# Kernel tuning notes

Measured on AMD Instinct MI355X. Metric: run time of the kernel, lower is better.

Reference implementation:

```python
import jax, jax.numpy as jnp
import numpy as np

ADAPTER_RATIO = 0.2


def setup_inputs() -> dict:
    key = jax.random.key(0)
    k1, k2, k3, k4, k5 = jax.random.split(key, 5)
    B, D, R, N_DOM, N_TXT = 16384, 1024, 256, 3, 1380
    image_features = jax.random.normal(k1, (B, D), dtype=jnp.float32)
    domain_labels = jax.random.randint(k2, (B,), 0, N_DOM, dtype=jnp.int64)
    W1 = jax.random.normal(k3, (N_DOM, D, R), dtype=jnp.float32) * 0.02
    W2 = jax.random.normal(k4, (N_DOM, R, D), dtype=jnp.float32) * 0.02
    txt = jax.random.normal(k5, (N_TXT, D), dtype=jnp.float32)
    # text features are L2-normalized at module init (encode_text then norm)
    text_features = txt / jnp.linalg.norm(txt, axis=-1, keepdims=True)
    logit_scale = jnp.asarray(np.log(1.0 / 0.07), dtype=jnp.float32)  # CLIP init
    return {
        "image_features": image_features,
        "domain_labels": domain_labels,
        "W1": W1,
        "W2": W2,
        "text_features": text_features,
        "logit_scale": logit_scale,
    }


def reference(image_features, domain_labels, W1, W2, text_features, logit_scale):
    # Domain-routed adapter MLP: run all n_domains experts (n is tiny), then
    # select the routed output per sample (equivalent to the per-sample loop).
    h = jax.nn.relu(jnp.einsum("bd,ndr->bnr", image_features, W1))  # [B,n,R]
    a = jax.nn.relu(jnp.einsum("bnr,nrd->bnd", h, W2))              # [B,n,D]
    idx = domain_labels[:, None, None]                                # [B,1,1]
    adapter_features = jnp.take_along_axis(a, idx, axis=1)[:, 0, :]   # [B,D]
    fused = ADAPTER_RATIO * adapter_features + (1.0 - ADAPTER_RATIO) * image_features
    fused = fused / jnp.linalg.norm(fused, axis=-1, keepdims=True)
    # text_features already normalized; concat over domains done upstream: [N_TXT, D]
    logits = jnp.exp(logit_scale) * (fused @ text_features.T)         # [B, N_TXT]
    return logits
```

## Files before the change

### kernel.cpp

```cpp
#include <hip/hip_runtime.h>
#include <hip/hip_bf16.h>
#include <math.h>

using bf16 = __hip_bfloat16;
typedef __attribute__((ext_vector_type(8))) short bf16x8;
typedef __attribute__((ext_vector_type(4))) float f32x4;
typedef __attribute__((ext_vector_type(4))) unsigned short us4;

#define GAS __attribute__((address_space(1)))
#define LAS __attribute__((address_space(3)))

__device__ __forceinline__ void gload_lds16(const bf16* g, bf16* lds) {
  __builtin_amdgcn_global_load_lds((const GAS void*)g, (LAS void*)lds, 16, 0, 0);
}
__device__ __forceinline__ float b2f(unsigned short u) {
  union { unsigned short s; bf16 b; } x; x.s = u; return __bfloat162float(x.b);
}

__global__ __launch_bounds__(256) void hist_k(const int* __restrict__ lab,
                                              int* __restrict__ blockHist) {
  const int blk = blockIdx.x, t = threadIdx.x;
  const int lane = t & 63, w = t >> 6;
  const int d = lab[blk * 256 + t];
  __shared__ int wc[4][3];
#pragma unroll
  for (int dd = 0; dd < 3; ++dd) {
    unsigned long long m = __ballot(d == dd);
    if (lane == 0) wc[w][dd] = __popcll(m);
  }
  __syncthreads();
  if (t < 3) blockHist[blk * 3 + t] = wc[0][t] + wc[1][t] + wc[2][t] + wc[3][t];
}

__global__ __launch_bounds__(256) void scan_k(const int* __restrict__ blockHist,
                                              int* __restrict__ blockOff,
                                              int* __restrict__ meta) {
  __shared__ int h[64][3];
  __shared__ int tot[3];
  const int t = threadIdx.x;
  if (t < 192) h[t / 3][t % 3] = blockHist[t];
  __syncthreads();
  if (t < 3) {
    int s = 0;
    for (int b = 0; b < 64; ++b) { int v = h[b][t]; h[b][t] = s; s += v; }
    tot[t] = s;
    meta[t] = s;
  }
  __syncthreads();
  if (t == 0) { meta[4] = 0; meta[5] = tot[0]; meta[6] = tot[0] + tot[1]; }
  if (t < 192) {
    int b = t / 3, d = t % 3;
    int base = (d == 0) ? 0 : (d == 1 ? tot[0] : tot[0] + tot[1]);
    blockOff[t] = base + h[b][d];
  }
}

__global__ __launch_bounds__(256) void scatter2_k(const int* __restrict__ lab,
                                                  const int* __restrict__ blockOff,
                                                  int* __restrict__ perm,
                                                  int* __restrict__ iperm) {
  const int blk = blockIdx.x, t = threadIdx.x;
  const int lane = t & 63, w = t >> 6;
  const int i = blk * 256 + t;
  const int d = lab[i];
  __shared__ int wc[4][3];
  unsigned long long mymask = 0;
#pragma unroll
  for (int dd = 0; dd < 3; ++dd) {
    unsigned long long m = __ballot(d == dd);
    if (lane == 0) wc[w][dd] = __popcll(m);
    if (dd == d) mymask = m;
  }
  __syncthreads();
  int woff = 0;
  for (int ww = 0; ww < w; ++ww) woff += wc[ww][d];
  const unsigned long long lt = ((unsigned long long)1 << lane) - 1;
  const int rank = blockOff[blk * 3 + d] + woff + __popcll(mymask & lt);
  perm[rank] = i;
  iperm[i] = rank;
}

__global__ __launch_bounds__(256) void cvt_all_k(const float* __restrict__ x,
                                                 const float* __restrict__ txt,
                                                 const int* __restrict__ iperm,
                                                 bf16* __restrict__ Xbc,
                                                 bf16* __restrict__ Tb) {
  const int nx = 16384 * 1024 / 4;
  const int ntext = 1536 * 1024;
  const int total = nx + ntext;
  for (int i = blockIdx.x * 256 + threadIdx.x; i < total; i += 2048 * 256) {
    if (i < nx) {
      const int row = i >> 8, c4 = i & 255;
      float4 v = ((const float4*)x)[i];
      bf16 t[4] = {__float2bfloat16(v.x), __float2bfloat16(v.y),
                   __float2bfloat16(v.z), __float2bfloat16(v.w)};
      ((us4*)Xbc)[(size_t)iperm[row] * 256 + c4] = *(const us4*)t;
    } else {
      int jj = i - nx;
      Tb[jj] = (jj < 1380 * 1024) ? __float2bfloat16(txt[jj]) : __float2bfloat16(0.f);
    }
  }
}

__global__ __launch_bounds__(256) void tr_wt_k(const float* __restrict__ W1,
                                               const float* __restrict__ W2,
                                               bf16* __restrict__ W1T,
                                               bf16* __restrict__ W2T) {
  __shared__ float s[64][65];
  int b = blockIdx.x;
  const float* W; bf16* WT; int R, C;
  if (b < 192) { W = W1; WT = W1T; R = 1024; C = 256; }
  else         { b -= 192; W = W2; WT = W2T; R = 256; C = 1024; }
  const int d = b / 64, tb = b % 64;
  const int tilesPerRow = C / 64;
  const int r0 = (tb / tilesPerRow) * 64;
  const int c0 = (tb % tilesPerRow) * 64;
  const float* Wd = W + (size_t)d * R * C;
  bf16* WTd = WT + (size_t)d * R * C;
  const int tx = threadIdx.x & 63, ty = threadIdx.x >> 6;
#pragma unroll
  for (int i = 0; i < 16; ++i)
    s[ty + i * 4][tx] = Wd[(size_t)(r0 + ty + i * 4) * C + c0 + tx];
  __syncthreads();
#pragma unroll
  for (int i = 0; i < 16; ++i)
    WTd[(size_t)(c0 + ty + i * 4) * R + r0 + tx] = __float2bfloat16(s[tx][ty + i * 4]);
}

template <int EPI, int NBLK>
__global__ __launch_bounds__(256) void gemm_bt(
    const bf16* __restrict__ A, const bf16* __restrict__ BT, bf16* __restrict__ Cv,
    const int* __restrict__ meta, int N, int K, int ldc, int Nvalid,
    const bf16* __restrict__ xb, float* __restrict__ ssp) {
  const int bid = blockIdx.x;
  const int xcd = bid & 7;
  const int seq = bid >> 3;
  const int nblkidx = seq % NBLK;
  const int dm = xcd + 8 * (seq / NBLK);
  const int dom = dm >> 7;
  const int mblk = dm & 127;

  const int cnt = meta[dom];
  const int base = meta[4 + dom];
  BT += (size_t)dom * N * K;

  const int m0 = mblk * 128;
  if (m0 >= cnt) return;
  const int n0 = nblkidx * 128;

  __shared__ bf16 sA[2][128][32];
  __shared__ bf16 sB[2][128][32];

  const int tid = threadIdx.x;
  const int wid = tid >> 6;
  const int lane = tid & 63;

  const int srow = (wid << 4) + (lane >> 2);
  const int skoff = (((lane & 3) ^ ((lane >> 2) & 3)) << 3);

  int p0 = m0 + srow;       if (p0 > cnt - 1) p0 = cnt - 1;
  int p1 = m0 + srow + 64;  if (p1 > cnt - 1) p1 = cnt - 1;
  const bf16* a0 = A + (size_t)(base + p0) * K + skoff;
  const bf16* a1 = A + (size_t)(base + p1) * K + skoff;
  const bf16* b0 = BT + (size_t)(n0 + srow) * K + skoff;
  const bf16* b1 = BT + (size_t)(n0 + srow + 64) * K + skoff;

  const int fr = lane & 15;
  const int fq = lane >> 4;
  const int rchunk = (fq ^ (fr & 3)) << 3;

  f32x4 acc[4][4];
#pragma unroll
  for (int m = 0; m < 4; ++m)
#pragma unroll
    for (int n = 0; n < 4; ++n) acc[m][n] = (f32x4){0.f, 0.f, 0.f, 0.f};

  const int nk = K >> 5;
  auto stage = [&](int buf, int kt) {
    gload_lds16(a0 + kt * 32, &sA[buf][wid * 16][0]);
    gload_lds16(a1 + kt * 32, &sA[buf][wid * 16 + 64][0]);
    gload_lds16(b0 + kt * 32, &sB[buf][wid * 16][0]);
    gload_lds16(b1 + kt * 32, &sB[buf][wid * 16 + 64][0]);
  };

  stage(0, 0);
  __syncthreads();
  const int wr = wid >> 1, wc = wid & 1;
  for (int kt = 0; kt < nk; ++kt) {
    const int cur = kt & 1;
    if (kt + 1 < nk) stage(cur ^ 1, kt + 1);
    bf16x8 af[4], bfr[4];
#pragma unroll
    for (int m = 0; m < 4; ++m)
      af[m] = *(const bf16x8*)&sA[cur][wr * 64 + m * 16 + fr][rchunk];
#pragma unroll
    for (int n = 0; n < 4; ++n)
      bfr[n] = *(const bf16x8*)&sB[cur][wc * 64 + n * 16 + fr][rchunk];
#pragma unroll
    for (int m = 0; m < 4; ++m)
#pragma unroll
      for (int n = 0; n < 4; ++n)
        acc[m][n] = __builtin_amdgcn_mfma_f32_16x16x32_bf16(af[m], bfr[n], acc[m][n], 0, 0, 0);
    __syncthreads();
  }

  if (EPI == 0) {
#pragma unroll
    for (int m = 0; m < 4; ++m) {
#pragma unroll
      for (int r = 0; r < 4; ++r) {
        const int p = m0 + wr * 64 + m * 16 + fq * 4 + r;
        if (p < cnt) {
          const size_t crow = (size_t)(base + p);
#pragma unroll
          for (int n = 0; n < 4; ++n) {
            const int col = n0 + wc * 64 + n * 16 + fr;
            if (col < Nvalid)
              Cv[crow * (size_t)ldc + col] = __float2bfloat16(fmaxf(acc[m][n][r], 0.f));
          }
        }
      }
    }
  } else {
    __shared__ float ssred[128][2];
#pragma unroll
    for (int m = 0; m < 4; ++m) {
#pragma unroll
      for (int r = 0; r < 4; ++r) {
        const int lr = wr * 64 + m * 16 + fq * 4 + r;
        const int p = m0 + lr;
        float rowss = 0.f;
        if (p < cnt) {
          const size_t crow = (size_t)(base + p);
#pragma unroll
          for (int n = 0; n < 4; ++n) {
            const int col = n0 + wc * 64 + n * 16 + fr;
            const float g = 0.2f * fmaxf(acc[m][n][r], 0.f) +
                            0.8f * b2f(*(const unsigned short*)&xb[crow * 1024 + col]);
            Cv[crow * (size_t)ldc + col] = __float2bfloat16(g);
            rowss += g * g;
          }
        }
        rowss += __shfl_xor(rowss, 1, 16);
        rowss += __shfl_xor(rowss, 2, 16);
        rowss += __shfl_xor(rowss, 4, 16);
        rowss += __shfl_xor(rowss, 8, 16);
        if (fr == 0) ssred[lr][wc] = rowss;
      }
    }
    __syncthreads();
    if (tid < 128) {
      const int p = m0 + tid;
      if (p < cnt)
        ssp[(size_t)nblkidx * 16384 + base + p] = ssred[tid][0] + ssred[tid][1];
    }
  }
}

__global__ __launch_bounds__(256, 2) void gemm3_cnt(
    const bf16* __restrict__ A, const bf16* __restrict__ BT,
    float* __restrict__ C, const float* __restrict__ scale_ptr,
    const float* __restrict__ ssp, const int* __restrict__ perm) {
  extern __shared__ bf16 smem[];
  bf16* sA0 = smem;
  bf16* sB0 = smem + 16384;

  const int tid = threadIdx.x;
  const int lane = tid & 63, wid = tid >> 6;
  const int wr = wid >> 1, wc = wid & 1;
  const int fr = lane & 15, fq = lane >> 4;

  const int bid = blockIdx.x;
  const int x = bid & 7, seq = bid >> 3;
  const int mb = x * 16 + (seq >> 3), nb = seq & 7;
  const int m0 = mb << 7, n0 = nb * 192;

  auto STAGE = [&](int t) {
    const int s = t & 1, koff = t << 6;
    bf16* da = sA0 + (s << 13);
#pragma unroll
    for (int L = 0; L < 4; ++L) {
      const int idx = (L << 8) + tid;
      const int r = idx >> 3, c = idx & 7;
      gload_lds16(A + (size_t)(m0 + r) * 1024 + koff + ((c ^ (r & 7)) << 3),
                  da + ((idx & ~63) << 3));
    }
    bf16* db = sB0 + s * 12288;
#pragma unroll
    for (int L = 0; L < 6; ++L) {
      const int idx = (L << 8) + tid;
      const int r = idx >> 3, c = idx & 7;
      gload_lds16(BT + (size_t)(n0 + r) * 1024 + koff + ((c ^ (r & 7)) << 3),
                  db + ((idx & ~63) << 3));
    }
  };
  auto LDA = [&](int s, int kk, bf16x8* dst) {
    const bf16* base = sA0 + (s << 13);
#pragma unroll
    for (int m = 0; m < 4; ++m) {
      const int row = (wr << 6) + (m << 4) + fr;
      dst[m] = *(const bf16x8*)(base + (row << 6) + ((((kk << 2) + fq) ^ (fr & 7)) << 3));
    }
  };
  auto LDB = [&](int s, int kk, bf16x8* dst) {
    const bf16* base = sB0 + s * 12288;
#pragma unroll
    for (int n = 0; n < 6; ++n) {
      const int row = wc * 96 + (n << 4) + fr;
      dst[n] = *(const bf16x8*)(base + (row << 6) + ((((kk << 2) + fq) ^ (fr & 7)) << 3));
    }
  };

  f32x4 acc[4][6];
#pragma unroll
  for (int m = 0; m < 4; ++m)
#pragma unroll
    for (int n = 0; n < 6; ++n) acc[m][n] = (f32x4){0.f, 0.f, 0.f, 0.f};

  STAGE(0); STAGE(1);
  asm volatile("s_waitcnt vmcnt(10)" ::: "memory");
  __builtin_amdgcn_s_barrier();

  const int nt = 16;
  for (int t = 0; t < nt; ++t) {
    const int s = t & 1;
    bf16x8 a0[4], a1[4], b0[6], b1[6];
    LDA(s, 0, a0); LDB(s, 0, b0);
    LDA(s, 1, a1); LDB(s, 1, b1);
    asm volatile("s_waitcnt lgkmcnt(0)" ::: "memory");
    __builtin_amdgcn_sched_barrier(0);
    __builtin_amdgcn_s_barrier();
    __builtin_amdgcn_sched_barrier(0);
    if (t + 2 < nt) STAGE(t + 2);
    __builtin_amdgcn_s_setprio(1);
#pragma unroll
    for (int m = 0; m < 4; ++m)
#pragma unroll
      for (int n = 0; n < 6; ++n)
        acc[m][n] = __builtin_amdgcn_mfma_f32_16x16x32_bf16(a0[m], b0[n], acc[m][n], 0, 0, 0);
#pragma unroll
    for (int m = 0; m < 4; ++m)
#pragma unroll
      for (int n = 0; n < 6; ++n)
        acc[m][n] = __builtin_amdgcn_mfma_f32_16x16x32_bf16(a1[m], b1[n], acc[m][n], 0, 0, 0);
    __builtin_amdgcn_s_setprio(0);
    if (t + 2 < nt) {
      asm volatile("s_waitcnt vmcnt(10)" ::: "memory");
    } else if (t + 1 < nt) {
      asm volatile("s_waitcnt vmcnt(0)" ::: "memory");
    }
    __builtin_amdgcn_sched_barrier(0);
    __builtin_amdgcn_s_barrier();
    __builtin_amdgcn_sched_barrier(0);
  }

  float* rlds = (float*)smem;
  int*   plds = (int*)((char*)smem + 512);
  if (tid < 128) {
    float s = 0.f;
#pragma unroll
    for (int b = 0; b < 8; ++b) s += ssp[b * 16384 + m0 + tid];
    rlds[tid] = rsqrtf(s);
    plds[tid] = perm[m0 + tid];
  }
  __syncthreads();

  const float sc = expf(*scale_ptr);
#pragma unroll
  for (int m = 0; m < 4; ++m) {
    const int lrow = (wr << 6) + (m << 4) + (fq << 2);
#pragma unroll
    for (int r = 0; r < 4; ++r) {
      const float rv = sc * rlds[lrow + r];
      const size_t orow = (size_t)plds[lrow + r];
#pragma unroll
      for (int n = 0; n < 6; ++n) {
        const int gcol = n0 + wc * 96 + (n << 4) + fr;
        if (gcol < 1380) C[orow * 1380 + gcol] = acc[m][n][r] * rv;
      }
    }
  }
}

extern "C" void kernel_launch(void* const* d_in, const int* in_sizes, int n_in,
                              void* d_out, int out_size, void* d_ws, size_t ws_size,
                              hipStream_t stream) {
  (void)in_sizes; (void)n_in; (void)out_size; (void)ws_size;
  const float* x    = (const float*)d_in[0];
  const int*   lab  = (const int*)d_in[1];
  const float* W1   = (const float*)d_in[2];
  const float* W2   = (const float*)d_in[3];
  const float* text = (const float*)d_in[4];
  const float* lsc  = (const float*)d_in[5];
  float* out = (float*)d_out;

  const int B = 16384, D = 1024, R = 256, NTP = 1536;

  char* p = (char*)d_ws;
  auto carve = [&](size_t bytes) {
    char* r = p;
    p += (bytes + 255) & ~(size_t)255;
    return r;
  };
  int*   meta  = (int*)carve(64);
  int*   bhist = (int*)carve(64 * 3 * 4);
  int*   boff  = (int*)carve(64 * 3 * 4);
  int*   perm  = (int*)carve((size_t)B * 4);
  int*   iperm = (int*)carve((size_t)B * 4);
  float* ssp   = (float*)carve((size_t)8 * B * 4);
  bf16*  Xbc   = (bf16*)carve((size_t)B * D * 2);
  bf16*  W1T   = (bf16*)carve((size_t)3 * R * D * 2);
  bf16*  W2T   = (bf16*)carve((size_t)3 * D * R * 2);
  bf16*  Tb    = (bf16*)carve((size_t)NTP * D * 2);
  bf16*  H     = (bf16*)carve((size_t)B * R * 2);
  bf16*  Fbc   = (bf16*)carve((size_t)B * D * 2);

  hist_k<<<B / 256, 256, 0, stream>>>(lab, bhist);
  scan_k<<<1, 256, 0, stream>>>(bhist, boff, meta);
  scatter2_k<<<B / 256, 256, 0, stream>>>(lab, boff, perm, iperm);

  cvt_all_k<<<2048, 256, 0, stream>>>(x, text, iperm, Xbc, Tb);
  tr_wt_k<<<384, 256, 0, stream>>>(W1, W2, W1T, W2T);

  gemm_bt<0, 2><<<768, 256, 0, stream>>>(
      Xbc, W1T, H, meta, R, D, R, R, nullptr, nullptr);
  gemm_bt<1, 8><<<3072, 256, 0, stream>>>(
      H, W2T, Fbc, meta, D, R, D, D, Xbc, ssp);
  gemm3_cnt<<<1024, 256, 81920, stream>>>(Fbc, Tb, out, lsc, ssp, perm);
}
```

Measured before the change: 154.5 us.

## Merge weight transpose into conversion kernel and widen GEMM K-tile to 64

Folds the weight transpose kernel into the input/text conversion kernel, so one launch does both and the per-launch overhead and serialization gap go away. Makes the K-tile of the grouped adapter GEMMs a template parameter and sets it to 64. The LDS staging and XOR swizzle are generalized to the wider tile, and each synchronized step now issues two MFMA sub-steps. The aim is fewer barriers and more work per pipeline stage, at the cost of twice the LDS per block, which may reduce occupancy.

Result: no change. 152.1 us (-1.5%).

```diff
diff --git a/kernel.cpp b/kernel.cpp
--- a/kernel.cpp
+++ b/kernel.cpp
@@ -80,15 +80,41 @@
   iperm[i] = rank;
 }
 
-__global__ __launch_bounds__(256) void cvt_all_k(const float* __restrict__ x,
-                                                 const float* __restrict__ txt,
-                                                 const int* __restrict__ iperm,
-                                                 bf16* __restrict__ Xbc,
-                                                 bf16* __restrict__ Tb) {
+__global__ __launch_bounds__(256) void prep_k(const float* __restrict__ x,
+                                              const float* __restrict__ txt,
+                                              const float* __restrict__ W1,
+                                              const float* __restrict__ W2,
+                                              const int* __restrict__ iperm,
+                                              bf16* __restrict__ Xbc,
+                                              bf16* __restrict__ Tb,
+                                              bf16* __restrict__ W1T,
+                                              bf16* __restrict__ W2T) {
+  __shared__ float s[64][65];
+  if (blockIdx.x < 384) {
+    int b = blockIdx.x;
+    const float* W; bf16* WT; int R, C;
+    if (b < 192) { W = W1; WT = W1T; R = 1024; C = 256; }
+    else         { b -= 192; W = W2; WT = W2T; R = 256; C = 1024; }
+    const int d = b / 64, tb = b % 64;
+    const int tilesPerRow = C / 64;
+    const int r0 = (tb / tilesPerRow) * 64;
+    const int c0 = (tb % tilesPerRow) * 64;
+    const float* Wd = W + (size_t)d * R * C;
+    bf16* WTd = WT + (size_t)d * R * C;
+    const int tx = threadIdx.x & 63, ty = threadIdx.x >> 6;
+#pragma unroll
+    for (int i = 0; i < 16; ++i)
+      s[ty + i * 4][tx] = Wd[(size_t)(r0 + ty + i * 4) * C + c0 + tx];
+    __syncthreads();
+#pragma unroll
+    for (int i = 0; i < 16; ++i)
+      WTd[(size_t)(c0 + ty + i * 4) * R + r0 + tx] = __float2bfloat16(s[tx][ty + i * 4]);
+    return;
+  }
   const int nx = 16384 * 1024 / 4;
   const int ntext = 1536 * 1024;
   const int total = nx + ntext;
-  for (int i = blockIdx.x * 256 + threadIdx.x; i < total; i += 2048 * 256) {
+  for (int i = (blockIdx.x - 384) * 256 + threadIdx.x; i < total; i += 2048 * 256) {
     if (i < nx) {
       const int row = i >> 8, c4 = i & 255;
       float4 v = ((const float4*)x)[i];
@@ -102,32 +128,7 @@
   }
 }
 
-__global__ __launch_bounds__(256) void tr_wt_k(const float* __restrict__ W1,
-                                               const float* __restrict__ W2,
-                                               bf16* __restrict__ W1T,
-                                               bf16* __restrict__ W2T) {
-  __shared__ float s[64][65];
-  int b = blockIdx.x;
-  const float* W; bf16* WT; int R, C;
-  if (b < 192) { W = W1; WT = W1T; R = 1024; C = 256; }
-  else         { b -= 192; W = W2; WT = W2T; R = 256; C = 1024; }
-  const int d = b / 64, tb = b % 64;
-  const int tilesPerRow = C / 64;
-  const int r0 = (tb / tilesPerRow) * 64;
-  const int c0 = (tb % tilesPerRow) * 64;
-  const float* Wd = W + (size_t)d * R * C;
-  bf16* WTd = WT + (size_t)d * R * C;
-  const int tx = threadIdx.x & 63, ty = threadIdx.x >> 6;
-#pragma unroll
-  for (int i = 0; i < 16; ++i)
-    s[ty + i * 4][tx] = Wd[(size_t)(r0 + ty + i * 4) * C + c0 + tx];
-  __syncthreads();
-#pragma unroll
-  for (int i = 0; i < 16; ++i)
-    WTd[(size_t)(c0 + ty + i * 4) * R + r0 + tx] = __float2bfloat16(s[tx][ty + i * 4]);
-}
-
-template <int EPI, int NBLK>
+template <int EPI, int NBLK, int BK>
 __global__ __launch_bounds__(256) void gemm_bt(
     const bf16* __restrict__ A, const bf16* __restrict__ BT, bf16* __restrict__ Cv,
     const int* __restrict__ meta, int N, int K, int ldc, int Nvalid,
@@ -148,26 +149,34 @@
   if (m0 >= cnt) return;
   const int n0 = nblkidx * 128;
 
-  __shared__ bf16 sA[2][128][32];
-  __shared__ bf16 sB[2][128][32];
+  constexpr int CH = BK / 8;
+  __shared__ bf16 sA[2][128][BK];
+  __shared__ bf16 sB[2][128][BK];
 
   const int tid = threadIdx.x;
   const int wid = tid >> 6;
   const int lane = tid & 63;
-
-  const int srow = (wid << 4) + (lane >> 2);
-  const int skoff = (((lane & 3) ^ ((lane >> 2) & 3)) << 3);
-
-  int p0 = m0 + srow;       if (p0 > cnt - 1) p0 = cnt - 1;
-  int p1 = m0 + srow + 64;  if (p1 > cnt - 1) p1 = cnt - 1;
-  const bf16* a0 = A + (size_t)(base + p0) * K + skoff;
-  const bf16* a1 = A + (size_t)(base + p1) * K + skoff;
-  const bf16* b0 = BT + (size_t)(n0 + srow) * K + skoff;
-  const bf16* b1 = BT + (size_t)(n0 + srow + 64) * K + skoff;
-
   const int fr = lane & 15;
   const int fq = lane >> 4;
-  const int rchunk = (fq ^ (fr & 3)) << 3;
+
+  auto stage = [&](int buf, int kt) {
+    const int koff = kt * BK;
+#pragma unroll
+    for (int L = 0; L < CH / 2; ++L) {
+      const int idx = L * 256 + tid;
+      const int r = idx / CH, c = idx % CH;
+      int ar = m0 + r; if (ar > cnt - 1) ar = cnt - 1;
+      gload_lds16(A + (size_t)(base + ar) * K + koff + ((c ^ (r & (CH - 1))) << 3),
+                  &sA[buf][0][0] + ((idx & ~63) << 3));
+    }
+#pragma unroll
+    for (int L = 0; L < CH / 2; ++L) {
+      const int idx = L * 256 + tid;
+      const int r = idx / CH, c = idx % CH;
+      gload_lds16(BT + (size_t)(n0 + r) * K + koff + ((c ^ (r & (CH - 1))) << 3),
+                  &sB[buf][0][0] + ((idx & ~63) << 3));
+    }
+  };
 
   f32x4 acc[4][4];
 #pragma unroll
@@ -175,32 +184,29 @@
 #pragma unroll
     for (int n = 0; n < 4; ++n) acc[m][n] = (f32x4){0.f, 0.f, 0.f, 0.f};
 
-  const int nk = K >> 5;
-  auto stage = [&](int buf, int kt) {
-    gload_lds16(a0 + kt * 32, &sA[buf][wid * 16][0]);
-    gload_lds16(a1 + kt * 32, &sA[buf][wid * 16 + 64][0]);
-    gload_lds16(b0 + kt * 32, &sB[buf][wid * 16][0]);
-    gload_lds16(b1 + kt * 32, &sB[buf][wid * 16 + 64][0]);
-  };
-
+  const int nk = K / BK;
   stage(0, 0);
   __syncthreads();
   const int wr = wid >> 1, wc = wid & 1;
   for (int kt = 0; kt < nk; ++kt) {
     const int cur = kt & 1;
     if (kt + 1 < nk) stage(cur ^ 1, kt + 1);
-    bf16x8 af[4], bfr[4];
-#pragma unroll
-    for (int m = 0; m < 4; ++m)
-      af[m] = *(const bf16x8*)&sA[cur][wr * 64 + m * 16 + fr][rchunk];
-#pragma unroll
-    for (int n = 0; n < 4; ++n)
-      bfr[n] = *(const bf16x8*)&sB[cur][wc * 64 + n * 16 + fr][rchunk];
-#pragma unroll
-    for (int m = 0; m < 4; ++m)
+#pragma unroll
+    for (int kk = 0; kk < BK / 32; ++kk) {
+      const int rchunk = (((kk << 2) + fq) ^ (fr & (CH - 1))) << 3;
+      bf16x8 af[4], bfr[4];
+#pragma unroll
+      for (int m = 0; m < 4; ++m)
+        af[m] = *(const bf16x8*)&sA[cur][wr * 64 + m * 16 + fr][0 + rchunk];
 #pragma unroll
       for (int n = 0; n < 4; ++n)
-        acc[m][n] = __builtin_amdgcn_mfma_f32_16x16x32_bf16(af[m], bfr[n], acc[m][n], 0, 0, 0);
+        bfr[n] = *(const bf16x8*)&sB[cur][wc * 64 + n * 16 + fr][0 + rchunk];
+#pragma unroll
+      for (int m = 0; m < 4; ++m)
+#pragma unroll
+        for (int n = 0; n < 4; ++n)
+          acc[m][n] = __builtin_amdgcn_mfma_f32_16x16x32_bf16(af[m], bfr[n], acc[m][n], 0, 0, 0);
+    }
     __syncthreads();
   }
 
@@ -419,12 +425,11 @@
   scan_k<<<1, 256, 0, stream>>>(bhist, boff, meta);
   scatter2_k<<<B / 256, 256, 0, stream>>>(lab, boff, perm, iperm);
 
-  cvt_all_k<<<2048, 256, 0, stream>>>(x, text, iperm, Xbc, Tb);
-  tr_wt_k<<<384, 256, 0, stream>>>(W1, W2, W1T, W2T);
-
-  gemm_bt<0, 2><<<768, 256, 0, stream>>>(
+  prep_k<<<384 + 2048, 256, 0, stream>>>(x, text, W1, W2, iperm, Xbc, Tb, W1T, W2T);
+
+  gemm_bt<0, 2, 64><<<768, 256, 0, stream>>>(
       Xbc, W1T, H, meta, R, D, R, R, nullptr, nullptr);
-  gemm_bt<1, 8><<<3072, 256, 0, stream>>>(
+  gemm_bt<1, 8, 64><<<3072, 256, 0, stream>>>(
       H, W2T, Fbc, meta, D, R, D, D, Xbc, ssp);
   gemm3_cnt<<<1024, 256, 81920, stream>>>(Fbc, Tb, out, lsc, ssp, perm);
 }
```
